# Optimization experiments

Hardware: AMD Instinct MI355X
Metric: run time of the kernel (lower is better)

The kernel has to match this reference:

```python
import jax, jax.numpy as jnp
import numpy as np

B, NC, NT = 16, 2048, 2048
IN_DIM, H_DIM, OUT_DIM = 128, 256, 256


def _mlp(x, w1, b1, w2, b2, w3, b3):
    # MLP(input_dim, [h, h], output_dim): Linear-ReLU-Linear-ReLU-Linear
    h = jax.nn.relu(x @ w1 + b1)
    h = jax.nn.relu(h @ w2 + b2)
    return h @ w3 + b3


def setup_inputs() -> dict:
    key = jax.random.key(0)
    ks = jax.random.split(key, 16)

    def lin(k, fan_in, fan_out):
        s = 1.0 / np.sqrt(fan_in)
        kw, kb = jax.random.split(k)
        w = jax.random.uniform(kw, (fan_in, fan_out), jnp.float32, -s, s)
        b = jax.random.uniform(kb, (fan_out,), jnp.float32, -s, s)
        return w, b

    qw1, qb1 = lin(ks[0], IN_DIM, H_DIM)
    qw2, qb2 = lin(ks[1], H_DIM, H_DIM)
    qw3, qb3 = lin(ks[2], H_DIM, OUT_DIM)
    kw1, kb1 = lin(ks[3], IN_DIM, H_DIM)
    kw2, kb2 = lin(ks[4], H_DIM, H_DIM)
    kw3, kb3 = lin(ks[5], H_DIM, OUT_DIM)

    return {
        "x_context": jax.random.normal(ks[6], (B, NC, IN_DIM), jnp.float32),
        "x_target": jax.random.normal(ks[7], (B, NT, IN_DIM), jnp.float32),
        "r_i": jax.random.normal(ks[8], (B, NC, OUT_DIM), jnp.float32),
        "qw1": qw1, "qb1": qb1, "qw2": qw2, "qb2": qb2, "qw3": qw3, "qb3": qb3,
        "kw1": kw1, "kb1": kb1, "kw2": kw2, "kb2": kb2, "kw3": kw3, "kb3": kb3,
    }


def reference(x_context, x_target, r_i,
              qw1, qb1, qw2, qb2, qw3, qb3,
              kw1, kb1, kw2, kb2, kw3, kb3):
    q = _mlp(x_target, qw1, qb1, qw2, qb2, qw3, qb3)   # [B, NT, D]
    k = _mlp(x_context, kw1, kb1, kw2, kb2, kw3, kb3)  # [B, NC, D]
    scale = jnp.sqrt(jnp.asarray(k.shape[-1], dtype=jnp.float32))
    w = jnp.einsum('btd,bcd->btc', q, k) / scale       # [B, NT, NC]
    # Faithful to torch.softmax(w, dim=1): normalize over the TARGET axis.
    w = jax.nn.softmax(w, axis=1)
    return jnp.einsum('btc,bcd->btd', w, r_i)          # [B, NT, OUT_DIM]
```

## Files before the change

kernel.cpp:

```cpp
#include <hip/hip_runtime.h>

#define BB 16
#define NT 2048
#define NC 2048
#define DIM 256
#define INDIM 128

typedef unsigned short u16;
typedef __bf16 bfx8 __attribute__((ext_vector_type(8)));
typedef __bf16 bfx8a __attribute__((ext_vector_type(8), aligned(8)));
typedef float f32x4 __attribute__((ext_vector_type(4)));

__device__ __forceinline__ u16 f2bf(float f) {
    union { float f; unsigned u; } v; v.f = f;
    return (u16)((v.u + 0x7FFFu + ((v.u >> 16) & 1u)) >> 16);
}

#define MFMA16(a, b, c) __builtin_amdgcn_mfma_f32_16x16x32_bf16((a), (b), (c), 0, 0, 0)


__global__ void cvt_w_all(const float* __restrict__ w0, const float* __restrict__ w1,
                          const float* __restrict__ w2, const float* __restrict__ w3,
                          const float* __restrict__ w4, const float* __restrict__ w5,
                          u16* __restrict__ o0, u16* __restrict__ o1, u16* __restrict__ o2,
                          u16* __restrict__ o3, u16* __restrict__ o4, u16* __restrict__ o5) {
    int bx = blockIdx.x;
    const float* src; u16* dst; int K, base;
    if (bx < 128)       { src = w0; dst = o0; K = 128; base = 0; }
    else if (bx < 384)  { src = w1; dst = o1; K = 256; base = 128; }
    else if (bx < 640)  { src = w2; dst = o2; K = 256; base = 384; }
    else if (bx < 768)  { src = w3; dst = o3; K = 128; base = 640; }
    else if (bx < 1024) { src = w4; dst = o4; K = 256; base = 768; }
    else                { src = w5; dst = o5; K = 256; base = 1024; }
    int idx = (bx - base) * 256 + threadIdx.x;
    int n = idx / K, k = idx - n * K;
    dst[idx] = f2bf(src[k * 256 + n]);
}

__global__ __launch_bounds__(256) void cvt_rt_kernel(const float* __restrict__ r, u16* __restrict__ rt) {
    __shared__ u16 t[64][68];
    int b = blockIdx.z;
    int c0 = blockIdx.x * 64, d0 = blockIdx.y * 64;
    int tid = threadIdx.x;
    const float* rb = r + (size_t)b * NC * DIM + d0;
    int cr = tid >> 4, df = (tid & 15) * 4;
#pragma unroll
    for (int p = 0; p < 4; p++) {
        int c = p * 16 + cr;
        float4 v = *reinterpret_cast<const float4*>(rb + (size_t)(c0 + c) * DIM + df);
        t[df + 0][c] = f2bf(v.x);
        t[df + 1][c] = f2bf(v.y);
        t[df + 2][c] = f2bf(v.z);
        t[df + 3][c] = f2bf(v.w);
    }
    __syncthreads();
    u16* rtb = rt + (size_t)b * DIM * NC;
    int dr = tid >> 3, cc = (tid & 7) * 8;
#pragma unroll
    for (int p = 0; p < 2; p++) {
        int d = p * 32 + dr;
        union { u16 u[8]; uint4 v; } pk;
#pragma unroll
        for (int j = 0; j < 8; j++) pk.u[j] = t[d][cc + j];
        *reinterpret_cast<uint4*>(rtb + (size_t)(d0 + d) * NC + c0 + cc) = pk.v;
    }
}


__global__ __launch_bounds__(256) void mlp_fused(const float* __restrict__ xq, const float* __restrict__ xk,
                                                 const u16* __restrict__ W1q, const u16* __restrict__ W1k,
                                                 const float* __restrict__ b1q, const float* __restrict__ b1k,
                                                 const u16* __restrict__ W2q, const u16* __restrict__ W2k,
                                                 const float* __restrict__ b2q, const float* __restrict__ b2k,
                                                 const u16* __restrict__ W3q, const u16* __restrict__ W3k,
                                                 const float* __restrict__ b3q, const float* __restrict__ b3k,
                                                 u16* __restrict__ oq, u16* __restrict__ ok) {
    __shared__ __align__(16) char lds[65536];
    char* h1 = lds;
    char* xa = lds + 32768;
    char* h2 = lds + 32768;

    int tid = threadIdx.x, lane = tid & 63, w = tid >> 6;
    int lr = lane & 15, lg = lane >> 4;
    int m0 = blockIdx.x * 64;
    bool isq = (blockIdx.y == 0);
    const float* X = (isq ? xq : xk) + (size_t)m0 * INDIM;
    const u16* W1 = isq ? W1q : W1k;  const float* b1 = isq ? b1q : b1k;
    const u16* W2 = isq ? W2q : W2k;  const float* b2 = isq ? b2q : b2k;
    const u16* W3 = isq ? W3q : W3k;  const float* b3 = isq ? b3q : b3k;
    u16* C = (isq ? oq : ok) + (size_t)m0 * 256;

#pragma unroll
    for (int j = 0; j < 4; j++) {
        int bo = (j * 256 + tid) * 16;
        int row = bo >> 8;
        int ir = bo & 255;
        const float* src = X + (size_t)row * INDIM + (ir >> 1);
        float4 f0 = *reinterpret_cast<const float4*>(src);
        float4 f1 = *reinterpret_cast<const float4*>(src + 4);
        union { u16 u[8]; uint4 v; } pk;
        pk.u[0] = f2bf(f0.x); pk.u[1] = f2bf(f0.y); pk.u[2] = f2bf(f0.z); pk.u[3] = f2bf(f0.w);
        pk.u[4] = f2bf(f1.x); pk.u[5] = f2bf(f1.y); pk.u[6] = f2bf(f1.z); pk.u[7] = f2bf(f1.w);
        *reinterpret_cast<uint4*>(xa + row * 256 + (ir ^ ((row & 7) << 4))) = pk.v;
    }
    __syncthreads();

    int n0 = w * 64;
    const int key = (lr & 7) << 4;

    {
        f32x4 acc[4][4] = {};
#pragma unroll
        for (int ks = 0; ks < 4; ks++) {
            bfx8 b[4];
#pragma unroll
            for (int nt = 0; nt < 4; nt++)
                b[nt] = *reinterpret_cast<const bfx8*>(W1 + (size_t)(n0 + nt * 16 + lr) * 128 + ks * 32 + lg * 8);
#pragma unroll
            for (int mt = 0; mt < 4; mt++) {
                bfx8 a = *reinterpret_cast<const bfx8*>(xa + (mt * 16 + lr) * 256 + ((ks * 64 + lg * 16) ^ key));
#pragma unroll
                for (int nt = 0; nt < 4; nt++)
                    acc[mt][nt] = MFMA16(a, b[nt], acc[mt][nt]);
            }
        }
#pragma unroll
        for (int nt = 0; nt < 4; nt++) {
            int col = n0 + nt * 16 + lr;
            float bv = b1[col];
#pragma unroll
            for (int mt = 0; mt < 4; mt++) {
#pragma unroll
                for (int r = 0; r < 4; r++) {
                    int row = mt * 16 + lg * 4 + r;
                    float v = fmaxf(acc[mt][nt][r] + bv, 0.0f);
                    *(u16*)(h1 + row * 512 + ((col * 2) ^ ((row & 7) << 4))) = f2bf(v);
                }
            }
        }
    }
    __syncthreads();

    {
        f32x4 acc[4][4] = {};
#pragma unroll
        for (int ks = 0; ks < 8; ks++) {
            bfx8 b[4];
#pragma unroll
            for (int nt = 0; nt < 4; nt++)
                b[nt] = *reinterpret_cast<const bfx8*>(W2 + (size_t)(n0 + nt * 16 + lr) * 256 + ks * 32 + lg * 8);
#pragma unroll
            for (int mt = 0; mt < 4; mt++) {
                bfx8 a = *reinterpret_cast<const bfx8*>(h1 + (mt * 16 + lr) * 512 + ((ks * 64 + lg * 16) ^ key));
#pragma unroll
                for (int nt = 0; nt < 4; nt++)
                    acc[mt][nt] = MFMA16(a, b[nt], acc[mt][nt]);
            }
        }
#pragma unroll
        for (int nt = 0; nt < 4; nt++) {
            int col = n0 + nt * 16 + lr;
            float bv = b2[col];
#pragma unroll
            for (int mt = 0; mt < 4; mt++) {
#pragma unroll
                for (int r = 0; r < 4; r++) {
                    int row = mt * 16 + lg * 4 + r;
                    float v = fmaxf(acc[mt][nt][r] + bv, 0.0f);
                    *(u16*)(h2 + row * 512 + ((col * 2) ^ ((row & 7) << 4))) = f2bf(v);
                }
            }
        }
    }
    __syncthreads();

    {
        f32x4 acc[4][4] = {};
#pragma unroll
        for (int ks = 0; ks < 8; ks++) {
            bfx8 b[4];
#pragma unroll
            for (int nt = 0; nt < 4; nt++)
                b[nt] = *reinterpret_cast<const bfx8*>(W3 + (size_t)(n0 + nt * 16 + lr) * 256 + ks * 32 + lg * 8);
#pragma unroll
            for (int mt = 0; mt < 4; mt++) {
                bfx8 a = *reinterpret_cast<const bfx8*>(h2 + (mt * 16 + lr) * 512 + ((ks * 64 + lg * 16) ^ key));
#pragma unroll
                for (int nt = 0; nt < 4; nt++)
                    acc[mt][nt] = MFMA16(a, b[nt], acc[mt][nt]);
            }
        }
        u16* ot = (u16*)h1;
#pragma unroll
        for (int nt = 0; nt < 4; nt++) {
            int col = n0 + nt * 16 + lr;
            float bv = b3[col];
#pragma unroll
            for (int mt = 0; mt < 4; mt++) {
#pragma unroll
                for (int r = 0; r < 4; r++) {
                    int row = mt * 16 + lg * 4 + r;
                    ot[row * 256 + col] = f2bf(acc[mt][nt][r] + bv);
                }
            }
        }
        __syncthreads();
#pragma unroll
        for (int p = 0; p < 8; p++) {
            int idx = p * 256 + tid;
            int row = idx >> 5, ck = idx & 31;
            *reinterpret_cast<uint4*>(C + (size_t)row * 256 + ck * 8) =
                *reinterpret_cast<const uint4*>(ot + row * 256 + ck * 8);
        }
    }
}


__global__ __launch_bounds__(256) void stats_kernel(const u16* __restrict__ q,
                                                    const u16* __restrict__ k,
                                                    float2* __restrict__ gso) {
    int flat = blockIdx.x;
    int sw = (flat & 7) * 64 + (flat >> 3);
    int b = sw >> 5;
    int c0 = (sw & 31) * 64;
    int tid = threadIdx.x, lane = tid & 63, w = tid >> 6;
    int lr = lane & 15, lg = lane >> 4;
    const u16* qb = q + (size_t)b * NT * DIM;
    const u16* kb = k + (size_t)b * NC * DIM;
    const float A2 = 1.44269504f / 16.0f;

    bfx8 kf[4][8];
#pragma unroll
    for (int j = 0; j < 4; j++)
#pragma unroll
        for (int ks = 0; ks < 8; ks++)
            kf[j][ks] = *reinterpret_cast<const bfx8*>(kb + (size_t)(c0 + j * 16 + lr) * DIM + ks * 32 + lg * 8);

    float m_run[4], l_run[4];
#pragma unroll
    for (int j = 0; j < 4; j++) { m_run[j] = -1e30f; l_run[j] = 0.0f; }

    for (int ts = 0; ts < NT / 64; ts++) {
        int t0 = ts * 64 + w * 16;
        f32x4 acc[4] = {};
#pragma unroll
        for (int ks = 0; ks < 8; ks++) {
            bfx8 a = *reinterpret_cast<const bfx8*>(qb + (size_t)(t0 + lr) * DIM + ks * 32 + lg * 8);
#pragma unroll
            for (int j = 0; j < 4; j++)
                acc[j] = MFMA16(a, kf[j][ks], acc[j]);
        }
#pragma unroll
        for (int j = 0; j < 4; j++) {
            f32x4 a = acc[j];
            float mx = fmaxf(fmaxf(a[0], a[1]), fmaxf(a[2], a[3]));
            float mn = fmaxf(m_run[j], mx);
            float t = mn * A2;
            float sum = exp2f(fmaf(a[0], A2, -t)) + exp2f(fmaf(a[1], A2, -t)) +
                        exp2f(fmaf(a[2], A2, -t)) + exp2f(fmaf(a[3], A2, -t));
            l_run[j] = l_run[j] * exp2f(fmaf(m_run[j], A2, -t)) + sum;
            m_run[j] = mn;
        }
    }

#pragma unroll
    for (int j = 0; j < 4; j++) {
        float m = m_run[j], l = l_run[j];
#pragma unroll
        for (int d = 16; d < 64; d <<= 1) {
            float mo = __shfl_xor(m, d);
            float lo = __shfl_xor(l, d);
            float mn = fmaxf(m, mo);
            l = l * exp2f((m - mn) * A2) + lo * exp2f((mo - mn) * A2);
            m = mn;
        }
        m_run[j] = m; l_run[j] = l;
    }

    __shared__ float sm[4][64], sl[4][64];
    if (lg == 0) {
#pragma unroll
        for (int j = 0; j < 4; j++) {
            sm[w][j * 16 + lr] = m_run[j];
            sl[w][j * 16 + lr] = l_run[j];
        }
    }
    __syncthreads();
    if (tid < 64) {
        float mf = sm[0][tid];
#pragma unroll
        for (int ww = 1; ww < 4; ww++) mf = fmaxf(mf, sm[ww][tid]);
        float lf = 0.0f;
#pragma unroll
        for (int ww = 0; ww < 4; ww++) lf += sl[ww][tid] * exp2f((sm[ww][tid] - mf) * A2);
        gso[(size_t)b * NC + c0 + tid] = make_float2(mf * A2, 1.0f / lf);
    }
}


__global__ __launch_bounds__(256, 2) void attn_kernel(const u16* __restrict__ q,
                                                      const u16* __restrict__ k,
                                                      const u16* __restrict__ rt,
                                                      const float2* __restrict__ gsg_,
                                                      float* __restrict__ out) {
    int flat = blockIdx.x;
    int sw = (flat & 7) * 64 + (flat >> 3);
    int b = sw >> 5;
    int t0 = (sw & 31) * 64;
    int tid = threadIdx.x, lane = tid & 63, w = tid >> 6;
    int lr = lane & 15, lg = lane >> 4;
    const u16* qb = q + (size_t)b * NT * DIM;
    const u16* kb = k + (size_t)b * NC * DIM;
    const u16* rtb = rt + (size_t)b * DIM * NC;

    __shared__ float2 gs[NC];
    __shared__ __align__(16) u16 kt[2][32 * 256];
    __shared__ __align__(16) u16 pl[64][40];

    {
        const float2* gsg = gsg_ + (size_t)b * NC;
        for (int i = tid; i < NC; i += 256) gs[i] = gsg[i];
    }
    __syncthreads();

#define STAGE(nb, cc) do {                                                          \
    const u16* ksrc_ = kb + (size_t)(cc) * DIM;                                     \
    _Pragma("unroll")                                                               \
    for (int i_ = 0; i_ < 4; i_++) {                                                \
        int off_ = ((w * 4 + i_) << 10) + (lane << 4);                              \
        int row_ = off_ >> 9;                                                       \
        int ss_  = ((off_ >> 4) & 31) ^ (row_ & 7);                                 \
        const u16* g_ = ksrc_ + row_ * DIM + ss_ * 8;                               \
        __builtin_amdgcn_global_load_lds(                                           \
            (const __attribute__((address_space(1))) void*)g_,                      \
            (__attribute__((address_space(3))) void*)(&kt[nb][(w * 4 + i_) << 9]),  \
            16, 0, 0);                                                              \
    }                                                                               \
} while (0)

    STAGE(0, 0);
    __builtin_amdgcn_sched_barrier(0);
    bfx8 rb_c[4], rb_n[4];
#pragma unroll
    for (int nt = 0; nt < 4; nt++)
        rb_c[nt] = *reinterpret_cast<const bfx8*>(rtb + (size_t)(w * 64 + nt * 16 + lr) * NC + lg * 8);
    bfx8 aq[8];
#pragma unroll
    for (int ks = 0; ks < 8; ks++)
        aq[ks] = *reinterpret_cast<const bfx8*>(qb + (size_t)(t0 + w * 16 + lr) * DIM + ks * 32 + lg * 8);
    __builtin_amdgcn_sched_barrier(0);
    asm volatile("s_waitcnt vmcnt(12)");
    __builtin_amdgcn_s_barrier();
    __builtin_amdgcn_sched_barrier(0);

    const float A = 1.44269504f / 16.0f;
    const int key = lr & 7;
    f32x4 acc[4][4] = {};
    int cur = 0;

    for (int c0 = 0; c0 < NC; c0 += 32) {
        const bool last = (c0 + 32 >= NC);
        if (!last) STAGE(cur ^ 1, c0 + 32);
        __builtin_amdgcn_sched_barrier(0);
        if (!last) {
#pragma unroll
            for (int nt = 0; nt < 4; nt++)
                rb_n[nt] = *reinterpret_cast<const bfx8*>(rtb + (size_t)(w * 64 + nt * 16 + lr) * NC + (c0 + 32) + lg * 8);
        }

        f32x4 s[2] = {};
        {
            const char* kc = (const char*)&kt[cur][0];
            __builtin_amdgcn_s_setprio(1);
#pragma unroll
            for (int ks = 0; ks < 8; ks++) {
                int slot = (ks << 2) | lg;
                bfx8 k0 = *reinterpret_cast<const bfx8*>(kc + (lr << 9) + (((slot ^ key)) << 4));
                bfx8 k1 = *reinterpret_cast<const bfx8*>(kc + ((16 + lr) << 9) + (((slot ^ key)) << 4));
                s[0] = MFMA16(aq[ks], k0, s[0]);
                s[1] = MFMA16(aq[ks], k1, s[1]);
            }
            __builtin_amdgcn_s_setprio(0);
        }
#pragma unroll
        for (int j = 0; j < 2; j++) {
            float2 g = gs[c0 + j * 16 + lr];
#pragma unroll
            for (int r = 0; r < 4; r++) {
                float p = exp2f(fmaf(s[j][r], A, -g.x)) * g.y;
                __bf16 h = (__bf16)p;
                pl[w * 16 + lg * 4 + r][j * 16 + lr] = *(u16*)&h;
            }
        }
        __builtin_amdgcn_sched_barrier(0);
        asm volatile("s_waitcnt lgkmcnt(0)");
        __builtin_amdgcn_s_barrier();
        __builtin_amdgcn_sched_barrier(0);

        __builtin_amdgcn_s_setprio(1);
#pragma unroll
        for (int mt = 0; mt < 4; mt++) {
            bfx8a pa = *reinterpret_cast<const bfx8a*>((const char*)pl + (mt * 16 + lr) * 80 + lg * 16);
#pragma unroll
            for (int nt = 0; nt < 4; nt++)
                acc[mt][nt] = MFMA16((bfx8)pa, rb_c[nt], acc[mt][nt]);
        }
        __builtin_amdgcn_s_setprio(0);

        __builtin_amdgcn_sched_barrier(0);
        asm volatile("s_waitcnt vmcnt(4) lgkmcnt(0)");
        __builtin_amdgcn_s_barrier();
        __builtin_amdgcn_sched_barrier(0);

#pragma unroll
        for (int nt = 0; nt < 4; nt++) rb_c[nt] = rb_n[nt];
        cur ^= 1;
    }
#undef STAGE

    float* ob = out + (size_t)b * NT * DIM;
#pragma unroll
    for (int nt = 0; nt < 4; nt++) {
        int col = w * 64 + nt * 16 + lr;
#pragma unroll
        for (int mt = 0; mt < 4; mt++) {
            int rowb = t0 + mt * 16 + lg * 4;
#pragma unroll
            for (int r = 0; r < 4; r++)
                ob[(size_t)(rowb + r) * DIM + col] = acc[mt][nt][r];
        }
    }
}


extern "C" void kernel_launch(void* const* d_in, const int* in_sizes, int n_in,
                              void* d_out, int out_size, void* d_ws, size_t ws_size,
                              hipStream_t stream) {
    const float* xc  = (const float*)d_in[0];
    const float* xt  = (const float*)d_in[1];
    const float* ri  = (const float*)d_in[2];
    const float* qw1 = (const float*)d_in[3];  const float* qb1 = (const float*)d_in[4];
    const float* qw2 = (const float*)d_in[5];  const float* qb2 = (const float*)d_in[6];
    const float* qw3 = (const float*)d_in[7];  const float* qb3 = (const float*)d_in[8];
    const float* kw1 = (const float*)d_in[9];  const float* kb1 = (const float*)d_in[10];
    const float* kw2 = (const float*)d_in[11]; const float* kb2 = (const float*)d_in[12];
    const float* kw3 = (const float*)d_in[13]; const float* kb3 = (const float*)d_in[14];

    if (ws_size < ((size_t)66 << 20)) return;

    char* ws = (char*)d_ws;
    u16* q   = (u16*)(ws);
    u16* kk  = (u16*)(ws + ((size_t)16 << 20));
    u16* rt  = (u16*)(ws + ((size_t)32 << 20));
    float2* gsb = (float2*)(ws + ((size_t)48 << 20));
    u16* wbuf = (u16*)(ws + ((size_t)48 << 20) + (512 << 10));
    u16* qw1t = wbuf;
    u16* qw2t = qw1t + 32768;
    u16* qw3t = qw2t + 65536;
    u16* kw1t = qw3t + 65536;
    u16* kw2t = kw1t + 32768;
    u16* kw3t = kw2t + 65536;

    cvt_w_all<<<dim3(1280), 256, 0, stream>>>(qw1, qw2, qw3, kw1, kw2, kw3,
                                              qw1t, qw2t, qw3t, kw1t, kw2t, kw3t);

    mlp_fused<<<dim3(512, 2), 256, 0, stream>>>(xt, xc,
                                                qw1t, kw1t, qb1, kb1,
                                                qw2t, kw2t, qb2, kb2,
                                                qw3t, kw3t, qb3, kb3,
                                                q, kk);

    cvt_rt_kernel<<<dim3(32, 4, BB), 256, 0, stream>>>(ri, rt);

    stats_kernel<<<dim3(512), 256, 0, stream>>>(q, kk, gsb);

    attn_kernel<<<dim3(512), 256, 0, stream>>>(q, kk, rt, gsb, (float*)d_out);
}
```

Baseline: 257.6 us.

## Double-buffer Q loads in stats kernel with lazy max rescale; shrink P padding

The softmax-statistics kernel now prefetches the next Q tile into registers while computing the current one, unrolled two steps per iteration. The running-max update only rescales when the new max exceeds the old by a threshold, which removes most per-step exp calls. In the attention kernel the P staging buffer row pitch goes from 40 to 36 elements, and the s_setprio hints around the MFMA blocks are removed. Risks: higher register pressure from the double buffer, a possible overflow margin issue with the lazy rescale, and LDS bank conflicts or misalignment with the new pitch.

```diff
diff --git a/kernel.cpp b/kernel.cpp
--- a/kernel.cpp
+++ b/kernel.cpp
@@ -240,28 +240,45 @@
 #pragma unroll
     for (int j = 0; j < 4; j++) { m_run[j] = -1e30f; l_run[j] = 0.0f; }
 
-    for (int ts = 0; ts < NT / 64; ts++) {
-        int t0 = ts * 64 + w * 16;
-        f32x4 acc[4] = {};
-#pragma unroll
-        for (int ks = 0; ks < 8; ks++) {
-            bfx8 a = *reinterpret_cast<const bfx8*>(qb + (size_t)(t0 + lr) * DIM + ks * 32 + lg * 8);
-#pragma unroll
-            for (int j = 0; j < 4; j++)
-                acc[j] = MFMA16(a, kf[j][ks], acc[j]);
-        }
-#pragma unroll
-        for (int j = 0; j < 4; j++) {
-            f32x4 a = acc[j];
-            float mx = fmaxf(fmaxf(a[0], a[1]), fmaxf(a[2], a[3]));
-            float mn = fmaxf(m_run[j], mx);
-            float t = mn * A2;
-            float sum = exp2f(fmaf(a[0], A2, -t)) + exp2f(fmaf(a[1], A2, -t)) +
-                        exp2f(fmaf(a[2], A2, -t)) + exp2f(fmaf(a[3], A2, -t));
-            l_run[j] = l_run[j] * exp2f(fmaf(m_run[j], A2, -t)) + sum;
-            m_run[j] = mn;
-        }
-    }
+#define LOADQ(dst, ts_) do {                                                        \
+    const u16* qrow_ = qb + (size_t)((ts_) * 64 + w * 16 + lr) * DIM;               \
+    _Pragma("unroll")                                                               \
+    for (int ks_ = 0; ks_ < 8; ks_++)                                               \
+        dst[ks_] = *reinterpret_cast<const bfx8*>(qrow_ + ks_ * 32 + lg * 8);       \
+} while (0)
+
+#define STEP(aq_) do {                                                              \
+    f32x4 sacc[4] = {};                                                             \
+    _Pragma("unroll")                                                               \
+    for (int ks_ = 0; ks_ < 8; ks_++) {                                             \
+        _Pragma("unroll")                                                           \
+        for (int j_ = 0; j_ < 4; j_++)                                              \
+            sacc[j_] = MFMA16(aq_[ks_], kf[j_][ks_], sacc[j_]);                     \
+    }                                                                               \
+    _Pragma("unroll")                                                               \
+    for (int j_ = 0; j_ < 4; j_++) {                                                \
+        f32x4 a_ = sacc[j_];                                                        \
+        float mx_ = fmaxf(fmaxf(a_[0], a_[1]), fmaxf(a_[2], a_[3]));                \
+        if (mx_ > m_run[j_] + 88.0f) {                                              \
+            l_run[j_] *= exp2f((m_run[j_] - mx_) * A2);                             \
+            m_run[j_] = mx_;                                                        \
+        }                                                                           \
+        float t_ = m_run[j_] * A2;                                                  \
+        l_run[j_] += exp2f(fmaf(a_[0], A2, -t_)) + exp2f(fmaf(a_[1], A2, -t_))      \
+                   + exp2f(fmaf(a_[2], A2, -t_)) + exp2f(fmaf(a_[3], A2, -t_));     \
+    }                                                                               \
+} while (0)
+
+    bfx8 a0[8], a1[8];
+    LOADQ(a0, 0);
+    for (int ts = 0; ts < NT / 64; ts += 2) {
+        LOADQ(a1, ts + 1);
+        STEP(a0);
+        if (ts + 2 < NT / 64) LOADQ(a0, ts + 2);
+        STEP(a1);
+    }
+#undef LOADQ
+#undef STEP
 
 #pragma unroll
     for (int j = 0; j < 4; j++) {
@@ -315,7 +332,7 @@
 
     __shared__ float2 gs[NC];
     __shared__ __align__(16) u16 kt[2][32 * 256];
-    __shared__ __align__(16) u16 pl[64][40];
+    __shared__ u16 pl[64][36];
 
     {
         const float2* gsg = gsg_ + (size_t)b * NC;
@@ -371,7 +388,6 @@
         f32x4 s[2] = {};
         {
             const char* kc = (const char*)&kt[cur][0];
-            __builtin_amdgcn_s_setprio(1);
 #pragma unroll
             for (int ks = 0; ks < 8; ks++) {
                 int slot = (ks << 2) | lg;
@@ -380,7 +396,6 @@
                 s[0] = MFMA16(aq[ks], k0, s[0]);
                 s[1] = MFMA16(aq[ks], k1, s[1]);
             }
-            __builtin_amdgcn_s_setprio(0);
         }
 #pragma unroll
         for (int j = 0; j < 2; j++) {
@@ -397,15 +412,13 @@
         __builtin_amdgcn_s_barrier();
         __builtin_amdgcn_sched_barrier(0);
 
-        __builtin_amdgcn_s_setprio(1);
 #pragma unroll
         for (int mt = 0; mt < 4; mt++) {
-            bfx8a pa = *reinterpret_cast<const bfx8a*>((const char*)pl + (mt * 16 + lr) * 80 + lg * 16);
+            bfx8a pa = *reinterpret_cast<const bfx8a*>((const char*)pl + (mt * 16 + lr) * 72 + lg * 16);
 #pragma unroll
             for (int nt = 0; nt < 4; nt++)
                 acc[mt][nt] = MFMA16((bfx8)pa, rb_c[nt], acc[mt][nt]);
         }
-        __builtin_amdgcn_s_setprio(0);
 
         __builtin_amdgcn_sched_barrier(0);
         asm volatile("s_waitcnt vmcnt(4) lgkmcnt(0)");
```

Result: faster. 251.4 us (-2.4%).
